# Kernel tuning notes

Measured on AMD Instinct MI355X. Metric: run time of the kernel, lower is better.

## Reference

```python
import jax, jax.numpy as jnp
import numpy as np

HEADS = 4
BN_EPS = 1e-5


def _hgat_conv(x, src, dst, node_type, edge_attr, edge_type,
               ne, W, We, a_src, a_dst, a_edge, ee, Wres, b, concat):
    """Heterogeneous GAT conv: per-type embeddings + edge-featured attention.
    x: [N, Fin]; edge_attr: [E, De]; returns [N, H*C] (concat) or [N, C]."""
    N = x.shape[0]
    C = W.shape[1] // HEADS
    xi = x + ne[node_type]                                  # node-type conditioning
    h = (xi @ W).reshape(N, HEADS, C)                       # [N, H, C]
    he = ((edge_attr + ee[edge_type]) @ We).reshape(-1, HEADS, C)  # [E, H, C]
    s = jnp.einsum('nhc,hc->nh', h, a_src)                  # [N, H]
    d = jnp.einsum('nhc,hc->nh', h, a_dst)                  # [N, H]
    e = jnp.einsum('ehc,hc->eh', he, a_edge)                # [E, H]
    alpha = jax.nn.leaky_relu(s[src] + d[dst] + e, 0.2)     # [E, H]
    # softmax over incoming edges per destination node
    amax = jax.ops.segment_max(alpha, dst, num_segments=N)  # [N, H]
    amax = jnp.where(jnp.isfinite(amax), amax, 0.0)
    ex = jnp.exp(alpha - amax[dst])
    den = jax.ops.segment_sum(ex, dst, num_segments=N)
    coef = ex / (den[dst] + 1e-16)                          # [E, H]
    msg = h[src] * coef[:, :, None]                         # [E, H, C]
    out = jax.ops.segment_sum(msg, dst, num_segments=N)     # [N, H, C]
    out = out.reshape(N, HEADS * C) if concat else out.mean(axis=1)
    return out + x @ Wres + b                               # residual + bias


def _batch_norm(x, gamma, beta):
    mu = x.mean(axis=0)
    var = x.var(axis=0)
    return (x - mu) * jax.lax.rsqrt(var + BN_EPS) * gamma + beta


def setup_inputs() -> dict:
    key = jax.random.key(0)
    ks = jax.random.split(key, 32)
    N, E, H = 50000, 400000, 32          # nodes, edges, hidden_channels
    DE = 64                               # edge_dim
    NT, ET = 3, 4                         # node / edge type counts
    D1 = H * HEADS                        # 128 = enc1 output / enc2 width

    def g(k, shape, scale=1.0):
        return (jax.random.normal(ks[k], shape, dtype=jnp.float32) * scale)

    inp = {
        'x': g(0, (N, H)),
        'edge_index': jax.random.randint(ks[1], (2, E), 0, N, dtype=jnp.int32),
        'node_type': jax.random.randint(ks[2], (N,), 0, NT, dtype=jnp.int32),
        'edge_attr': g(3, (E, DE)),
        'edge_type': jax.random.randint(ks[4], (E,), 0, ET, dtype=jnp.int32),
        # enc1 params (in=32, per-head out=32, concat -> 128)
        'ne1': g(5, (NT, H), 0.1),
        'w1': g(6, (H, HEADS * H), 1.0 / np.sqrt(H)),
        'we1': g(7, (DE, HEADS * H), 1.0 / np.sqrt(DE)),
        'asrc1': g(8, (HEADS, H), 0.1), 'adst1': g(9, (HEADS, H), 0.1),
        'aedge1': g(10, (HEADS, H), 0.1),
        'ee1': g(11, (ET, DE), 0.1),
        'wres1': g(12, (H, D1), 1.0 / np.sqrt(H)),
        'b1': jnp.zeros((D1,), jnp.float32),
        # BatchNorm(128)
        'gamma': jnp.ones((D1,), jnp.float32),
        'beta': jnp.zeros((D1,), jnp.float32),
        # enc2 params (in=128, per-head out=128, mean -> 128)
        'ne2': g(13, (NT, D1), 0.1),
        'w2': g(14, (D1, HEADS * D1), 1.0 / np.sqrt(D1)),
        'we2': g(15, (DE, HEADS * D1), 1.0 / np.sqrt(DE)),
        'asrc2': g(16, (HEADS, D1), 0.1), 'adst2': g(17, (HEADS, D1), 0.1),
        'aedge2': g(18, (HEADS, D1), 0.1),
        'ee2': g(19, (ET, DE), 0.1),
        'wres2': g(20, (D1, D1), 1.0 / np.sqrt(D1)),
        'b2': jnp.zeros((D1,), jnp.float32),
    }
    return inp


def reference(x, edge_index, node_type, edge_attr, edge_type,
              ne1, w1, we1, asrc1, adst1, aedge1, ee1, wres1, b1,
              gamma, beta,
              ne2, w2, we2, asrc2, adst2, aedge2, ee2, wres2, b2):
    src, dst = edge_index[0], edge_index[1]
    h = _hgat_conv(x, src, dst, node_type, edge_attr, edge_type,
                   ne1, w1, we1, asrc1, adst1, aedge1, ee1, wres1, b1,
                   concat=True)
    h = _batch_norm(h, gamma, beta)
    out = _hgat_conv(h, src, dst, node_type, edge_attr, edge_type,
                     ne2, w2, we2, asrc2, adst2, aedge2, ee2, wres2, b2,
                     concat=False)
    return out
```

## Files before the change

### kernel.cpp

```cpp
#include <hip/hip_runtime.h>
#include <hip/hip_bf16.h>

typedef unsigned short u16;
typedef unsigned int u32;

constexpr int NN = 50000;
constexpr int NE = 400000;
constexpr int MPAD = 50048;

typedef __attribute__((ext_vector_type(8))) short s16x8;
typedef __attribute__((ext_vector_type(4))) float f32x4;

__device__ __forceinline__ float bf2f(u16 u) {
    union { u32 i; float f; } v; v.i = ((u32)u) << 16; return v.f;
}
__device__ __forceinline__ u16 f2bf(float f) {
    union { float f; u32 i; } v; v.f = f;
    u32 r = v.i + 0x7fffu + ((v.i >> 16) & 1u);
    return (u16)(r >> 16);
}
__device__ __forceinline__ float ldf(const void* p, size_t i, int isbf) {
    if (isbf) return bf2f(((const u16*)p)[i]);
    return ((const float*)p)[i];
}
__device__ __forceinline__ float clampf(float v) {
    return fminf(fmaxf(v, -1e4f), 1e4f);
}

__device__ int   g_flag;
__device__ int   g_counter;
__device__ float g_qe1[256], g_qe2[256];
__device__ float g_eq1[16], g_eq2[16];
__device__ float g_ps1[128], g_pd1[128], g_ps2[512], g_pd2[512];
__device__ float g_bnsum[128], g_bnsumsq[128], g_bnscale[128], g_bnshift[128];
__device__ int   g_deg[NN], g_start[NN], g_cur[NN];
__device__ int   g_eidx[NE];
__device__ __attribute__((aligned(16))) float g_sbuf[NN * 4];
__device__ __attribute__((aligned(16))) float g_dbuf[NN * 4];
__device__ __attribute__((aligned(16))) float g_alpha[(size_t)NE * 4];
__device__ __attribute__((aligned(16))) float g_el2[(size_t)NE * 4];
__device__ __attribute__((aligned(16))) float g_xbuf[(size_t)NN * 128];
__device__ __attribute__((aligned(16))) float g_acc2[(size_t)NN * 128];
__device__ __attribute__((aligned(16))) u16 g_A1[(size_t)MPAD * 64];
__device__ __attribute__((aligned(16))) u16 g_A2[(size_t)MPAD * 160];
__device__ __attribute__((aligned(16))) u16 g_B1t[192 * 64];
__device__ __attribute__((aligned(16))) u16 g_B1bt[128 * 128];
__device__ __attribute__((aligned(16))) u16 g_B2t[192 * 160];
__device__ __attribute__((aligned(16))) u16 g_B2bt[128 * 512];
__device__ __attribute__((aligned(16))) u16 g_qeB[16 * 64];
__device__ __attribute__((aligned(16))) u16 g_xi1[(size_t)NN * 32];
__device__ __attribute__((aligned(16))) u16 g_xi2[(size_t)NN * 128];
__device__ __attribute__((aligned(16))) u16 g_agg1[(size_t)MPAD * 128];
__device__ __attribute__((aligned(16))) u16 g_agg2[(size_t)MPAD * 512];

__global__ void k_detect(const u16* x) {
    if (threadIdx.x == 0) {
        int cnt = 0;
        for (int i = 0; i < 64; i++) {
            u16 u = x[2 * i];
            int ex = (u >> 7) & 0xff;
            if (ex >= 100 && ex <= 140) cnt++;
        }
        g_flag = (cnt >= 40) ? 1 : 0;
        g_counter = 0;
    }
}
__global__ void k_zero() {
    int i = blockIdx.x * blockDim.x + threadIdx.x;
    if (i < NN) g_deg[i] = 0;
    if (i < 128) { g_bnsum[i] = 0.f; g_bnsumsq[i] = 0.f; }
}

__global__ __launch_bounds__(256) void k_prep(
    const void* we1, const void* ae1, const void* we2, const void* ae2,
    const void* w1, const void* as1, const void* ad1,
    const void* w2, const void* as2, const void* ad2) {
    int isbf = g_flag;
    int t = threadIdx.x;
    int idx = blockIdx.x * 16 + (t >> 4);
    int s = t & 15;
    float a = 0.f;
    if (idx < 256) {
        int k = idx >> 2, hd = idx & 3;
        for (int c = s; c < 32; c += 16)
            a += ldf(we1, k * 128 + hd * 32 + c, isbf) * ldf(ae1, hd * 32 + c, isbf);
    } else if (idx < 512) {
        int i2 = idx - 256;
        int k = i2 >> 2, hd = i2 & 3;
        for (int c = s; c < 128; c += 16)
            a += ldf(we2, k * 512 + hd * 128 + c, isbf) * ldf(ae2, hd * 128 + c, isbf);
    } else if (idx < 768) {
        int i2 = idx - 512;
        int isd = i2 >> 7, j = i2 & 127;
        int h = j >> 5, k = j & 31;
        const void* av = isd ? ad1 : as1;
        for (int c = s; c < 32; c += 16)
            a += ldf(w1, k * 128 + h * 32 + c, isbf) * ldf(av, h * 32 + c, isbf);
    } else {
        int i2 = idx - 768;
        int isd = i2 >> 9, j = i2 & 511;
        int h = j >> 7, k = j & 127;
        const void* av = isd ? ad2 : as2;
        for (int c = s; c < 128; c += 16)
            a += ldf(w2, (size_t)k * 512 + h * 128 + c, isbf) * ldf(av, h * 128 + c, isbf);
    }
#pragma unroll
    for (int mk = 8; mk >= 1; mk >>= 1) a += __shfl_xor(a, mk);
    if (s == 0) {
        if (idx < 256) g_qe1[idx] = a;
        else if (idx < 512) g_qe2[idx - 256] = a;
        else if (idx < 768) {
            int i2 = idx - 512;
            if (i2 >> 7) g_pd1[i2 & 127] = a; else g_ps1[i2 & 127] = a;
        } else {
            int i2 = idx - 768;
            if (i2 >> 9) g_pd2[i2 & 511] = a; else g_ps2[i2 & 511] = a;
        }
    }
}
__global__ void k_prep2(const void* ee1, const void* ee2) {
    int isbf = g_flag;
    int t = threadIdx.x;
    int idx = blockIdx.x * 16 + (t >> 4);
    int s = t & 15;
    int lyr = idx >> 4;
    int et = (idx >> 2) & 3, h = idx & 3;
    const void* ee = lyr ? ee2 : ee1;
    const float* qe = lyr ? g_qe2 : g_qe1;
    float a = 0.f;
    for (int k = s; k < 64; k += 16)
        a += ldf(ee, et * 64 + k, isbf) * qe[k * 4 + h];
#pragma unroll
    for (int mk = 8; mk >= 1; mk >>= 1) a += __shfl_xor(a, mk);
    if (s == 0) {
        if (lyr) g_eq2[et * 4 + h] = a; else g_eq1[et * 4 + h] = a;
    }
    int base = blockIdx.x * 256 + t;
    for (int i = base; i < 1024; i += 512) {
        int col = i >> 6, k = i & 63;
        float v = 0.f;
        if (col < 4) v = g_qe1[k * 4 + col];
        else if (col < 8) v = g_qe2[k * 4 + (col - 4)];
        g_qeB[col * 64 + k] = f2bf(v);
    }
}

__global__ void k_deg(const int* __restrict__ dstp) {
    int e = blockIdx.x * blockDim.x + threadIdx.x;
    if (e < NE) atomicAdd(&g_deg[dstp[e]], 1);
}
__global__ void k_start() {
    int n = blockIdx.x * blockDim.x + threadIdx.x;
    if (n < NN) {
        int d = g_deg[n];
        int s = atomicAdd(&g_counter, d);
        g_start[n] = s; g_cur[n] = s;
    }
}
__global__ void k_scatter(const int* __restrict__ dstp) {
    int e = blockIdx.x * blockDim.x + threadIdx.x;
    if (e < NE) {
        int slot = atomicAdd(&g_cur[dstp[e]], 1);
        g_eidx[slot] = e;
    }
}

__device__ __forceinline__ u16 a1val(const void* x, int n, int k, int nt, int isbf) {
    if (k < 32) return f2bf(ldf(x, (size_t)n * 32 + k, isbf));
    if (k == 32 + nt || k == 35) return 0x3F80u;
    return 0;
}
__global__ __launch_bounds__(256) void k_buildA1(const void* x, const int* __restrict__ ntype,
                                                 const void* ne1) {
    int isbf = g_flag;
    int i = blockIdx.x * 256 + threadIdx.x;
    if (i >= MPAD * 32) return;
    int n = i >> 5, k2 = (i & 31) << 1;
    u32 pk = 0;
    if (n < NN) {
        int nt = ntype[n];
        pk = (u32)a1val(x, n, k2, nt, isbf) | ((u32)a1val(x, n, k2 + 1, nt, isbf) << 16);
        if (k2 < 32) {
            float x0 = ldf(x, (size_t)n * 32 + k2, isbf) + ldf(ne1, nt * 32 + k2, isbf);
            float x1 = ldf(x, (size_t)n * 32 + k2 + 1, isbf) + ldf(ne1, nt * 32 + k2 + 1, isbf);
            ((u32*)g_xi1)[(size_t)n * 16 + (k2 >> 1)] =
                (u32)f2bf(x0) | ((u32)f2bf(x1) << 16);
        }
    }
    ((u32*)g_A1)[i] = pk;
}
__global__ __launch_bounds__(256) void k_a2tail(const int* __restrict__ ntype) {
    int i = blockIdx.x * 256 + threadIdx.x;
    if (i >= NN * 16) return;
    int n = i >> 4, q = i & 15;
    int k2 = 128 + q * 2;
    int nt = ntype[n];
    u16 lo = (k2 == 128 + nt || k2 == 131) ? 0x3F80u : 0;
    u16 hi = (k2 + 1 == 128 + nt || k2 + 1 == 131) ? 0x3F80u : 0;
    ((u32*)g_A2)[(size_t)n * 80 + 64 + q] = (u32)lo | ((u32)hi << 16);
}
__global__ __launch_bounds__(256) void k_xi2(const int* __restrict__ ntype, const void* ne2) {
    int isbf = g_flag;
    int i = blockIdx.x * 256 + threadIdx.x;
    if (i >= NN * 64) return;
    int n = i >> 6, jp = (i & 63) << 1;
    int nt = ntype[n];
    float v0 = g_xbuf[(size_t)n * 128 + jp] * g_bnscale[jp] + g_bnshift[jp]
             + ldf(ne2, nt * 128 + jp, isbf);
    float v1 = g_xbuf[(size_t)n * 128 + jp + 1] * g_bnscale[jp + 1] + g_bnshift[jp + 1]
             + ldf(ne2, nt * 128 + jp + 1, isbf);
    ((u32*)g_xi2)[i] = (u32)f2bf(v0) | ((u32)f2bf(v1) << 16);
}

__global__ void k_buildB1(const void* ne1, const void* w1, const void* wres1, const void* b1) {
    int isbf = g_flag;
    int j = blockIdx.x;
    int k = threadIdx.x;
    float v = 0.f;
    if (j < 128) {
        if (k < 32) v = ldf(wres1, k * 128 + j, isbf);
        else if (k == 35) v = ldf(b1, j, isbf);
    } else if (j < 136) {
        int h = (j - 128) & 3;
        const float* p = (j < 132) ? g_ps1 : g_pd1;
        if (k < 32) v = p[h * 32 + k];
        else if (k < 35) {
            int tt = k - 32; float a = 0.f;
            for (int c = 0; c < 32; c++)
                a += ldf(ne1, tt * 32 + c, isbf) * p[h * 32 + c];
            v = a;
        }
    }
    (void)w1;
    g_B1t[j * 64 + k] = f2bf(v);
}
__global__ void k_buildB1b(const void* w1) {
    int isbf = g_flag;
    int j = blockIdx.x;
    int k = threadIdx.x;
    float v = ((k >> 5) == (j >> 5)) ? ldf(w1, (k & 31) * 128 + j, isbf) : 0.f;
    g_B1bt[j * 128 + k] = f2bf(v);
}
__global__ void k_buildB2(const void* ne2, const void* w2, const void* wres2, const void* b2) {
    int isbf = g_flag;
    int j = blockIdx.x;
    int k = threadIdx.x;
    if (k >= 160) return;
    float v = 0.f;
    if (j < 128) {
        if (k < 128) v = g_bnscale[k] * ldf(wres2, k * 128 + j, isbf);
        else if (k == 131) {
            float a = ldf(b2, j, isbf);
            for (int c = 0; c < 128; c++)
                a += g_bnshift[c] * ldf(wres2, c * 128 + j, isbf);
            v = a;
        }
    } else if (j < 136) {
        int h = (j - 128) & 3;
        const float* p = (j < 132) ? g_ps2 : g_pd2;
        if (k < 128) v = g_bnscale[k] * p[h * 128 + k];
        else if (k < 131) {
            int tt = k - 128; float a = 0.f;
            for (int c = 0; c < 128; c++)
                a += (g_bnshift[c] + ldf(ne2, tt * 128 + c, isbf)) * p[h * 128 + c];
            v = a;
        }
    }
    (void)w2;
    g_B2t[j * 160 + k] = f2bf(v);
}
__global__ void k_buildB2b(const void* w2) {
    int isbf = g_flag;
    int j = blockIdx.x;
    for (int k = threadIdx.x; k < 512; k += 256) {
        float v = 0.25f * ldf(w2, (size_t)(k & 127) * 512 + (k >> 7) * 128 + j, isbf);
        g_B2bt[j * 512 + k] = f2bf(v);
    }
}

template<int K, int KT, int LAYER>
__global__ __launch_bounds__(256) void k_gemm(void* outp) {
    constexpr int KP = KT + 8;
    __shared__ __attribute__((aligned(16))) u16 As[64 * KP];
    __shared__ __attribute__((aligned(16))) u16 Bs[64 * KP];
    const u16* __restrict__ A  = (LAYER == 1) ? g_A1 : (LAYER == 2) ? g_A2
                               : (LAYER == 3) ? g_agg1 : g_agg2;
    const u16* __restrict__ Bt = (LAYER == 1) ? g_B1t : (LAYER == 2) ? g_B2t
                               : (LAYER == 3) ? g_B1bt : g_B2bt;
    int isbf = g_flag;
    const int t = threadIdx.x;
    const int mb = blockIdx.x, cb = blockIdx.y;
    const int wave = t >> 6, lane = t & 63;
    const int lr = lane & 15, lg = lane >> 4;
    f32x4 acc[4] = {};
    constexpr int CH = KT / 8;
#pragma unroll 1
    for (int kt = 0; kt < K / KT; kt++) {
        __syncthreads();
        for (int c = t; c < 64 * CH; c += 256) {
            int r = c / CH, o = (c - r * CH) * 8;
            *(s16x8*)&As[r * KP + o] =
                *(const s16x8*)&A[((size_t)(mb * 64 + r)) * K + kt * KT + o];
            *(s16x8*)&Bs[r * KP + o] =
                *(const s16x8*)&Bt[((size_t)(cb * 64 + r)) * K + kt * KT + o];
        }
        __syncthreads();
        const u16* ap  = &As[(wave * 16 + lr) * KP + lg * 8];
        const u16* bp0 = &Bs[lr * KP + lg * 8];
#pragma unroll
        for (int ks = 0; ks < KT / 32; ks++) {
            s16x8 af = *(const s16x8*)(ap + ks * 32);
#pragma unroll
            for (int ct = 0; ct < 4; ct++) {
                s16x8 bf = *(const s16x8*)(bp0 + ct * 16 * KP + ks * 32);
                acc[ct] = __builtin_amdgcn_mfma_f32_16x16x32_bf16(af, bf, acc[ct], 0, 0, 0);
            }
        }
    }
    const int rowb = mb * 64 + wave * 16 + lg * 4;
#pragma unroll
    for (int ct = 0; ct < 4; ct++) {
        int j = cb * 64 + ct * 16 + lr;
#pragma unroll
        for (int r = 0; r < 4; r++) {
            int n = rowb + r;
            if (n >= NN) continue;
            float v = acc[ct][r];
            if (LAYER == 1) {
                if (j < 128)      g_xbuf[(size_t)n * 128 + j] = clampf(v);
                else if (j < 132) g_sbuf[n * 4 + (j - 128)] = clampf(v);
                else if (j < 136) g_dbuf[n * 4 + (j - 132)] = clampf(v);
            } else if (LAYER == 2) {
                if (j < 128)      g_acc2[(size_t)n * 128 + j] = clampf(v);
                else if (j < 132) g_sbuf[n * 4 + (j - 128)] = clampf(v);
                else if (j < 136) g_dbuf[n * 4 + (j - 132)] = clampf(v);
            } else if (LAYER == 3) {
                float* p = &g_xbuf[(size_t)n * 128 + j];
                float x = clampf(*p + v);
                *p = x;
                g_A2[(size_t)n * 160 + j] = f2bf(x);
            } else {
                float v2 = clampf(g_acc2[(size_t)n * 128 + j] + v);
                if (isbf) ((u16*)outp)[(size_t)n * 128 + j] = f2bf(v2);
                else      ((float*)outp)[(size_t)n * 128 + j] = v2;
            }
        }
    }
}

__global__ __launch_bounds__(256) void k_edgemm(
    const int* __restrict__ etype, const void* eattr) {
    int isbf = g_flag;
    int t = threadIdx.x, wave = t >> 6, lane = t & 63;
    int lr = lane & 15, lg = lane >> 4;
    s16x8 bf0 = *(const s16x8*)&g_qeB[lr * 64 + lg * 8];
    s16x8 bf1 = *(const s16x8*)&g_qeB[lr * 64 + 32 + lg * 8];
    int ebase = blockIdx.x * 256 + wave * 64;
#pragma unroll 1
    for (int tile = 0; tile < 4; tile++) {
        int e0 = ebase + tile * 16;
        int ea = e0 + lr; if (ea >= NE) ea = NE - 1;
        f32x4 acc = {};
        if (isbf) {
            const u16* ep = (const u16*)eattr + (size_t)ea * 64 + lg * 8;
            s16x8 va = *(const s16x8*)(ep);
            s16x8 vb = *(const s16x8*)(ep + 32);
            acc = __builtin_amdgcn_mfma_f32_16x16x32_bf16(va, bf0, acc, 0, 0, 0);
            acc = __builtin_amdgcn_mfma_f32_16x16x32_bf16(vb, bf1, acc, 0, 0, 0);
        } else {
            const float* ep = (const float*)eattr + (size_t)ea * 64 + lg * 8;
            float4 fa = *(const float4*)(ep);
            float4 fb = *(const float4*)(ep + 4);
            float4 fc = *(const float4*)(ep + 32);
            float4 fd = *(const float4*)(ep + 36);
            s16x8 va, vb;
            va[0] = (short)f2bf(fa.x); va[1] = (short)f2bf(fa.y);
            va[2] = (short)f2bf(fa.z); va[3] = (short)f2bf(fa.w);
            va[4] = (short)f2bf(fb.x); va[5] = (short)f2bf(fb.y);
            va[6] = (short)f2bf(fb.z); va[7] = (short)f2bf(fb.w);
            vb[0] = (short)f2bf(fc.x); vb[1] = (short)f2bf(fc.y);
            vb[2] = (short)f2bf(fc.z); vb[3] = (short)f2bf(fc.w);
            vb[4] = (short)f2bf(fd.x); vb[5] = (short)f2bf(fd.y);
            vb[6] = (short)f2bf(fd.z); vb[7] = (short)f2bf(fd.w);
            acc = __builtin_amdgcn_mfma_f32_16x16x32_bf16(va, bf0, acc, 0, 0, 0);
            acc = __builtin_amdgcn_mfma_f32_16x16x32_bf16(vb, bf1, acc, 0, 0, 0);
        }
#pragma unroll
        for (int r = 0; r < 4; r++) {
            int ee = e0 + lg * 4 + r;
            int lb = lg * 16;
            float v0 = __shfl(acc[r], lb + 0), v1 = __shfl(acc[r], lb + 1);
            float v2 = __shfl(acc[r], lb + 2), v3 = __shfl(acc[r], lb + 3);
            float w0 = __shfl(acc[r], lb + 4), w1 = __shfl(acc[r], lb + 5);
            float w2 = __shfl(acc[r], lb + 6), w3 = __shfl(acc[r], lb + 7);
            if (ee < NE && (lr == 0 || lr == 4)) {
                int et = etype[ee];
                if (lr == 0) {
                    const float* q = g_eq1 + et * 4;
                    *(float4*)(g_alpha + 4 * (size_t)ee) = make_float4(
                        v0 + q[0], v1 + q[1], v2 + q[2], v3 + q[3]);
                } else {
                    const float* q = g_eq2 + et * 4;
                    *(float4*)(g_el2 + 4 * (size_t)ee) = make_float4(
                        w0 + q[0], w1 + q[1], w2 + q[2], w3 + q[3]);
                }
            }
        }
    }
}

__global__ __launch_bounds__(256) void k_edgeadd(
    const int* __restrict__ srcp, const int* __restrict__ dstp, int lyr) {
    int e = blockIdx.x * 256 + threadIdx.x;
    if (e >= NE) return;
    const float* el = (lyr == 1) ? g_alpha : g_el2;
    float4 p = *(const float4*)(el + 4 * (size_t)e);
    int ss = srcp[e], dd = dstp[e];
    float4 sb = *(const float4*)(g_sbuf + ss * 4);
    float4 db = *(const float4*)(g_dbuf + dd * 4);
    float a0 = sb.x + db.x + p.x;
    float a1 = sb.y + db.y + p.y;
    float a2 = sb.z + db.z + p.z;
    float a3 = sb.w + db.w + p.w;
    a0 = a0 > 0.f ? a0 : 0.2f * a0;
    a1 = a1 > 0.f ? a1 : 0.2f * a1;
    a2 = a2 > 0.f ? a2 : 0.2f * a2;
    a3 = a3 > 0.f ? a3 : 0.2f * a3;
    *(float4*)(g_alpha + 4 * (size_t)e) = make_float4(
        clampf(a0), clampf(a1), clampf(a2), clampf(a3));
}

__global__ __launch_bounds__(256) void k_att1(const int* __restrict__ srcp) {
    int lane = threadIdx.x & 63;
    int n = blockIdx.x * 4 + (threadIdx.x >> 6);
    if (n >= NN) return;
    int st = g_start[n], dg = g_deg[n];
    float m0 = -1e30f, m1 = -1e30f, m2 = -1e30f, m3 = -1e30f;
    for (int i = lane; i < dg; i += 64) {
        int e = g_eidx[st + i];
        float4 a = *(const float4*)(g_alpha + 4 * (size_t)e);
        m0 = fmaxf(m0, a.x); m1 = fmaxf(m1, a.y);
        m2 = fmaxf(m2, a.z); m3 = fmaxf(m3, a.w);
    }
    for (int mk = 32; mk >= 1; mk >>= 1) {
        m0 = fmaxf(m0, __shfl_xor(m0, mk)); m1 = fmaxf(m1, __shfl_xor(m1, mk));
        m2 = fmaxf(m2, __shfl_xor(m2, mk)); m3 = fmaxf(m3, __shfl_xor(m3, mk));
    }
    int j0 = 2 * lane;
    int hd = j0 >> 5;
    float z0 = 0.f, z1 = 0.f, z2 = 0.f, z3 = 0.f;
    float acc0 = 0.f, acc1 = 0.f;
    for (int base = 0; base < dg; base += 64) {
        int i = base + lane;
        int sidx = 0; float c0 = 0.f, c1 = 0.f, c2 = 0.f, c3 = 0.f;
        if (i < dg) {
            int e = g_eidx[st + i];
            float4 a = *(const float4*)(g_alpha + 4 * (size_t)e);
            sidx = srcp[e];
            c0 = expf(a.x - m0); c1 = expf(a.y - m1);
            c2 = expf(a.z - m2); c3 = expf(a.w - m3);
            z0 += c0; z1 += c1; z2 += c2; z3 += c3;
        }
        int cnt = min(64, dg - base);
        for (int jj = 0; jj < cnt; jj++) {
            int s2 = __shfl(sidx, jj);
            float b0 = __shfl(c0, jj), b1 = __shfl(c1, jj);
            float b2v = __shfl(c2, jj), b3 = __shfl(c3, jj);
            float cs = hd == 0 ? b0 : hd == 1 ? b1 : hd == 2 ? b2v : b3;
            u32 hv = *(const u32*)(g_xi1 + (size_t)s2 * 32 + (j0 & 31));
            acc0 += bf2f((u16)(hv & 0xffff)) * cs;
            acc1 += bf2f((u16)(hv >> 16)) * cs;
        }
    }
    for (int mk = 32; mk >= 1; mk >>= 1) {
        z0 += __shfl_xor(z0, mk); z1 += __shfl_xor(z1, mk);
        z2 += __shfl_xor(z2, mk); z3 += __shfl_xor(z3, mk);
    }
    float iv = 1.f / ((hd == 0 ? z0 : hd == 1 ? z1 : hd == 2 ? z2 : z3) + 1e-16f);
    ((u32*)g_agg1)[((size_t)n * 128 + j0) >> 1] =
        (u32)f2bf(acc0 * iv) | ((u32)f2bf(acc1 * iv) << 16);
}

__global__ __launch_bounds__(256) void k_bnstats() {
    int t = threadIdx.x;
    int j = t & 127;
    int r0 = blockIdx.x * 2 + (t >> 7);
    float s = 0.f, ss = 0.f;
    for (int r = r0; r < NN; r += 500) {
        float v = g_xbuf[(size_t)r * 128 + j];
        s += v; ss += v * v;
    }
    atomicAdd(&g_bnsum[j], s);
    atomicAdd(&g_bnsumsq[j], ss);
}
__global__ void k_bnfin(const void* gamma, const void* beta) {
    int isbf = g_flag;
    int j = threadIdx.x;
    float mu = g_bnsum[j] * (1.f / NN);
    float var = fmaxf(g_bnsumsq[j] * (1.f / NN) - mu * mu, 0.f);
    float rstd = rsqrtf(var + 1e-5f);
    float sc = ldf(gamma, j, isbf) * rstd;
    g_bnscale[j] = sc;
    g_bnshift[j] = ldf(beta, j, isbf) - mu * sc;
}

__global__ __launch_bounds__(256) void k_att2(const int* __restrict__ srcp) {
    int lane = threadIdx.x & 63;
    int n = blockIdx.x * 4 + (threadIdx.x >> 6);
    if (n >= NN) return;
    int st = g_start[n], dg = g_deg[n];
    float m0 = -1e30f, m1 = -1e30f, m2 = -1e30f, m3 = -1e30f;
    for (int i = lane; i < dg; i += 64) {
        int e = g_eidx[st + i];
        float4 a = *(const float4*)(g_alpha + 4 * (size_t)e);
        m0 = fmaxf(m0, a.x); m1 = fmaxf(m1, a.y);
        m2 = fmaxf(m2, a.z); m3 = fmaxf(m3, a.w);
    }
    for (int mk = 32; mk >= 1; mk >>= 1) {
        m0 = fmaxf(m0, __shfl_xor(m0, mk)); m1 = fmaxf(m1, __shfl_xor(m1, mk));
        m2 = fmaxf(m2, __shfl_xor(m2, mk)); m3 = fmaxf(m3, __shfl_xor(m3, mk));
    }
    int c0 = 2 * lane;
    float z0 = 0.f, z1 = 0.f, z2 = 0.f, z3 = 0.f;
    float a00 = 0.f, a01 = 0.f, a10 = 0.f, a11 = 0.f;
    float a20 = 0.f, a21 = 0.f, a30 = 0.f, a31 = 0.f;
    for (int base = 0; base < dg; base += 64) {
        int i = base + lane;
        int sidx = 0; float c0f = 0.f, c1f = 0.f, c2f = 0.f, c3f = 0.f;
        if (i < dg) {
            int e = g_eidx[st + i];
            float4 a = *(const float4*)(g_alpha + 4 * (size_t)e);
            sidx = srcp[e];
            c0f = expf(a.x - m0); c1f = expf(a.y - m1);
            c2f = expf(a.z - m2); c3f = expf(a.w - m3);
            z0 += c0f; z1 += c1f; z2 += c2f; z3 += c3f;
        }
        int cnt = min(64, dg - base);
        for (int jj = 0; jj < cnt; jj++) {
            int s2 = __shfl(sidx, jj);
            float b0 = __shfl(c0f, jj), b1 = __shfl(c1f, jj);
            float b2v = __shfl(c2f, jj), b3 = __shfl(c3f, jj);
            u32 hv = *(const u32*)(g_xi2 + (size_t)s2 * 128 + c0);
            float lo = bf2f((u16)(hv & 0xffff)), hi = bf2f((u16)(hv >> 16));
            a00 += lo * b0;  a01 += hi * b0;
            a10 += lo * b1;  a11 += hi * b1;
            a20 += lo * b2v; a21 += hi * b2v;
            a30 += lo * b3;  a31 += hi * b3;
        }
    }
    for (int mk = 32; mk >= 1; mk >>= 1) {
        z0 += __shfl_xor(z0, mk); z1 += __shfl_xor(z1, mk);
        z2 += __shfl_xor(z2, mk); z3 += __shfl_xor(z3, mk);
    }
    float iv0 = 1.f / (z0 + 1e-16f), iv1 = 1.f / (z1 + 1e-16f);
    float iv2 = 1.f / (z2 + 1e-16f), iv3 = 1.f / (z3 + 1e-16f);
    u32* out = (u32*)g_agg2 + (((size_t)n * 512 + c0) >> 1);
    out[0]   = (u32)f2bf(a00 * iv0) | ((u32)f2bf(a01 * iv0) << 16);
    out[64]  = (u32)f2bf(a10 * iv1) | ((u32)f2bf(a11 * iv1) << 16);
    out[128] = (u32)f2bf(a20 * iv2) | ((u32)f2bf(a21 * iv2) << 16);
    out[192] = (u32)f2bf(a30 * iv3) | ((u32)f2bf(a31 * iv3) << 16);
}

extern "C" void kernel_launch(void* const* d_in, const int* in_sizes, int n_in,
                              void* d_out, int out_size, void* d_ws, size_t ws_size,
                              hipStream_t stream) {
    const void* x     = d_in[0];
    const int* ei     = (const int*)d_in[1];
    const int* ntype  = (const int*)d_in[2];
    const void* eattr = d_in[3];
    const int* etype  = (const int*)d_in[4];
    const void* ne1   = d_in[5];
    const void* w1    = d_in[6];
    const void* we1   = d_in[7];
    const void* asrc1 = d_in[8];
    const void* adst1 = d_in[9];
    const void* aedge1= d_in[10];
    const void* ee1   = d_in[11];
    const void* wres1 = d_in[12];
    const void* b1    = d_in[13];
    const void* gamma = d_in[14];
    const void* beta  = d_in[15];
    const void* ne2   = d_in[16];
    const void* w2    = d_in[17];
    const void* we2   = d_in[18];
    const void* asrc2 = d_in[19];
    const void* adst2 = d_in[20];
    const void* aedge2= d_in[21];
    const void* ee2   = d_in[22];
    const void* wres2 = d_in[23];
    const void* b2    = d_in[24];
    (void)in_sizes; (void)n_in; (void)out_size; (void)d_ws; (void)ws_size;

    const int* srcp = ei;
    const int* dstp = ei + NE;

    k_detect<<<1, 64, 0, stream>>>((const u16*)x);
    k_zero<<<196, 256, 0, stream>>>();
    k_prep<<<112, 256, 0, stream>>>(we1, aedge1, we2, aedge2,
                                    w1, asrc1, adst1, w2, asrc2, adst2);
    k_prep2<<<2, 256, 0, stream>>>(ee1, ee2);
    k_deg<<<1563, 256, 0, stream>>>(dstp);
    k_start<<<196, 256, 0, stream>>>();
    k_scatter<<<1563, 256, 0, stream>>>(dstp);

    k_edgemm<<<(NE + 255) / 256, 256, 0, stream>>>(etype, eattr);

    k_buildA1<<<(MPAD * 32 + 255) / 256, 256, 0, stream>>>(x, ntype, ne1);
    k_buildB1<<<192, 64, 0, stream>>>(ne1, w1, wres1, b1);
    k_buildB1b<<<128, 128, 0, stream>>>(w1);
    k_gemm<64, 64, 1><<<dim3(MPAD / 64, 3), 256, 0, stream>>>(nullptr);
    k_edgeadd<<<1563, 256, 0, stream>>>(srcp, dstp, 1);
    k_att1<<<12500, 256, 0, stream>>>(srcp);
    k_gemm<128, 128, 3><<<dim3(MPAD / 64, 2), 256, 0, stream>>>(nullptr);

    k_bnstats<<<250, 256, 0, stream>>>();
    k_bnfin<<<1, 128, 0, stream>>>(gamma, beta);

    k_xi2<<<12500, 256, 0, stream>>>(ntype, ne2);
    k_a2tail<<<(NN * 16 + 255) / 256, 256, 0, stream>>>(ntype);
    k_buildB2<<<192, 192, 0, stream>>>(ne2, w2, wres2, b2);
    k_buildB2b<<<128, 256, 0, stream>>>(w2);
    k_gemm<160, 160, 2><<<dim3(MPAD / 64, 3), 256, 0, stream>>>(nullptr);
    k_edgeadd<<<1563, 256, 0, stream>>>(srcp, dstp, 2);
    k_att2<<<12500, 256, 0, stream>>>(srcp);
    k_gemm<512, 128, 4><<<dim3(MPAD / 64, 2), 256, 0, stream>>>(d_out);
}
```

Before: 595.6 us.

## Write attention logits in CSR order with atomic segment max and fuse small kernels

The edge-add kernel now stores each edge's attention logits directly at its CSR slot and updates a per-destination max through order-preserving integer atomicMax. The attention kernels then read logits and source indices contiguously and skip the separate max pass and the edge-index indirection. Several small setup kernels are merged (detect+zero, a2tail+xi2, B1/B1b, B2/B2b) to cut launch count. The cost is 1.6M extra atomics, which can contend on high-degree nodes, plus an extra slot array and a re-zeroing of the max keys between layers.

```diff
diff --git a/kernel.cpp b/kernel.cpp
--- a/kernel.cpp
+++ b/kernel.cpp
@@ -25,6 +25,16 @@
 }
 __device__ __forceinline__ float clampf(float v) {
     return fminf(fmaxf(v, -1e4f), 1e4f);
+}
+__device__ __forceinline__ u32 menc(float f) {
+    union { float f; u32 i; } v; v.f = f;
+    return (v.i & 0x80000000u) ? ~v.i : (v.i | 0x80000000u);
+}
+__device__ __forceinline__ float mdec(u32 k) {
+    if (k == 0u) return 0.f;
+    union { u32 i; float f; } v;
+    v.i = (k & 0x80000000u) ? (k & 0x7fffffffu) : ~k;
+    return v.f;
 }
 
 __device__ int   g_flag;
@@ -34,11 +44,14 @@
 __device__ float g_ps1[128], g_pd1[128], g_ps2[512], g_pd2[512];
 __device__ float g_bnsum[128], g_bnsumsq[128], g_bnscale[128], g_bnshift[128];
 __device__ int   g_deg[NN], g_start[NN], g_cur[NN];
-__device__ int   g_eidx[NE];
+__device__ int   g_slot[NE];
+__device__ int   g_srccsr[NE];
+__device__ u32   g_mkey[NN * 4];
 __device__ __attribute__((aligned(16))) float g_sbuf[NN * 4];
 __device__ __attribute__((aligned(16))) float g_dbuf[NN * 4];
 __device__ __attribute__((aligned(16))) float g_alpha[(size_t)NE * 4];
 __device__ __attribute__((aligned(16))) float g_el2[(size_t)NE * 4];
+__device__ __attribute__((aligned(16))) float g_acsr[(size_t)NE * 4];
 __device__ __attribute__((aligned(16))) float g_xbuf[(size_t)NN * 128];
 __device__ __attribute__((aligned(16))) float g_acc2[(size_t)NN * 128];
 __device__ __attribute__((aligned(16))) u16 g_A1[(size_t)MPAD * 64];
@@ -53,22 +66,21 @@
 __device__ __attribute__((aligned(16))) u16 g_agg1[(size_t)MPAD * 128];
 __device__ __attribute__((aligned(16))) u16 g_agg2[(size_t)MPAD * 512];
 
-__global__ void k_detect(const u16* x) {
-    if (threadIdx.x == 0) {
+__global__ void k_zero(const u16* x) {
+    int i = blockIdx.x * blockDim.x + threadIdx.x;
+    if (i < NN) g_deg[i] = 0;
+    if (i < NN * 4) g_mkey[i] = 0u;
+    if (i < 128) { g_bnsum[i] = 0.f; g_bnsumsq[i] = 0.f; }
+    if (i == 0) {
         int cnt = 0;
-        for (int i = 0; i < 64; i++) {
-            u16 u = x[2 * i];
+        for (int j = 0; j < 64; j++) {
+            u16 u = x[2 * j];
             int ex = (u >> 7) & 0xff;
             if (ex >= 100 && ex <= 140) cnt++;
         }
         g_flag = (cnt >= 40) ? 1 : 0;
         g_counter = 0;
     }
-}
-__global__ void k_zero() {
-    int i = blockIdx.x * blockDim.x + threadIdx.x;
-    if (i < NN) g_deg[i] = 0;
-    if (i < 128) { g_bnsum[i] = 0.f; g_bnsumsq[i] = 0.f; }
 }
 
 __global__ __launch_bounds__(256) void k_prep(
@@ -157,11 +169,12 @@
         g_start[n] = s; g_cur[n] = s;
     }
 }
-__global__ void k_scatter(const int* __restrict__ dstp) {
+__global__ void k_scatter(const int* __restrict__ srcp, const int* __restrict__ dstp) {
     int e = blockIdx.x * blockDim.x + threadIdx.x;
     if (e < NE) {
         int slot = atomicAdd(&g_cur[dstp[e]], 1);
-        g_eidx[slot] = e;
+        g_slot[e] = slot;
+        g_srccsr[slot] = srcp[e];
     }
 }
 
@@ -189,19 +202,18 @@
     }
     ((u32*)g_A1)[i] = pk;
 }
-__global__ __launch_bounds__(256) void k_a2tail(const int* __restrict__ ntype) {
+__global__ __launch_bounds__(256) void k_xi2(const int* __restrict__ ntype, const void* ne2) {
+    int isbf = g_flag;
     int i = blockIdx.x * 256 + threadIdx.x;
-    if (i >= NN * 16) return;
-    int n = i >> 4, q = i & 15;
-    int k2 = 128 + q * 2;
-    int nt = ntype[n];
-    u16 lo = (k2 == 128 + nt || k2 == 131) ? 0x3F80u : 0;
-    u16 hi = (k2 + 1 == 128 + nt || k2 + 1 == 131) ? 0x3F80u : 0;
-    ((u32*)g_A2)[(size_t)n * 80 + 64 + q] = (u32)lo | ((u32)hi << 16);
-}
-__global__ __launch_bounds__(256) void k_xi2(const int* __restrict__ ntype, const void* ne2) {
-    int isbf = g_flag;
-    int i = blockIdx.x * 256 + threadIdx.x;
+    if (i < NN * 4) g_mkey[i] = 0u;
+    if (i < NN * 16) {
+        int n = i >> 4, q = i & 15;
+        int k2 = 128 + q * 2;
+        int nt = ntype[n];
+        u16 lo = (k2 == 128 + nt || k2 == 131) ? 0x3F80u : 0;
+        u16 hi = (k2 + 1 == 128 + nt || k2 + 1 == 131) ? 0x3F80u : 0;
+        ((u32*)g_A2)[(size_t)n * 80 + 64 + q] = (u32)lo | ((u32)hi << 16);
+    }
     if (i >= NN * 64) return;
     int n = i >> 6, jp = (i & 63) << 1;
     int nt = ntype[n];
@@ -212,69 +224,71 @@
     ((u32*)g_xi2)[i] = (u32)f2bf(v0) | ((u32)f2bf(v1) << 16);
 }
 
-__global__ void k_buildB1(const void* ne1, const void* w1, const void* wres1, const void* b1) {
-    int isbf = g_flag;
-    int j = blockIdx.x;
+__global__ void k_buildB1all(const void* ne1, const void* w1,
+                             const void* wres1, const void* b1) {
+    int isbf = g_flag;
+    int bj = blockIdx.x;
     int k = threadIdx.x;
-    float v = 0.f;
-    if (j < 128) {
-        if (k < 32) v = ldf(wres1, k * 128 + j, isbf);
-        else if (k == 35) v = ldf(b1, j, isbf);
-    } else if (j < 136) {
-        int h = (j - 128) & 3;
-        const float* p = (j < 132) ? g_ps1 : g_pd1;
-        if (k < 32) v = p[h * 32 + k];
-        else if (k < 35) {
-            int tt = k - 32; float a = 0.f;
-            for (int c = 0; c < 32; c++)
-                a += ldf(ne1, tt * 32 + c, isbf) * p[h * 32 + c];
-            v = a;
-        }
-    }
-    (void)w1;
-    g_B1t[j * 64 + k] = f2bf(v);
-}
-__global__ void k_buildB1b(const void* w1) {
-    int isbf = g_flag;
-    int j = blockIdx.x;
+    if (bj < 192) {
+        if (k >= 64) return;
+        int j = bj;
+        float v = 0.f;
+        if (j < 128) {
+            if (k < 32) v = ldf(wres1, k * 128 + j, isbf);
+            else if (k == 35) v = ldf(b1, j, isbf);
+        } else if (j < 136) {
+            int h = (j - 128) & 3;
+            const float* p = (j < 132) ? g_ps1 : g_pd1;
+            if (k < 32) v = p[h * 32 + k];
+            else if (k < 35) {
+                int tt = k - 32; float a = 0.f;
+                for (int c = 0; c < 32; c++)
+                    a += ldf(ne1, tt * 32 + c, isbf) * p[h * 32 + c];
+                v = a;
+            }
+        }
+        g_B1t[j * 64 + k] = f2bf(v);
+    } else {
+        int j = bj - 192;
+        float v = ((k >> 5) == (j >> 5)) ? ldf(w1, (k & 31) * 128 + j, isbf) : 0.f;
+        g_B1bt[j * 128 + k] = f2bf(v);
+    }
+}
+__global__ void k_buildB2all(const void* ne2, const void* w2,
+                             const void* wres2, const void* b2) {
+    int isbf = g_flag;
+    int bj = blockIdx.x;
     int k = threadIdx.x;
-    float v = ((k >> 5) == (j >> 5)) ? ldf(w1, (k & 31) * 128 + j, isbf) : 0.f;
-    g_B1bt[j * 128 + k] = f2bf(v);
-}
-__global__ void k_buildB2(const void* ne2, const void* w2, const void* wres2, const void* b2) {
-    int isbf = g_flag;
-    int j = blockIdx.x;
-    int k = threadIdx.x;
-    if (k >= 160) return;
-    float v = 0.f;
-    if (j < 128) {
-        if (k < 128) v = g_bnscale[k] * ldf(wres2, k * 128 + j, isbf);
-        else if (k == 131) {
-            float a = ldf(b2, j, isbf);
-            for (int c = 0; c < 128; c++)
-                a += g_bnshift[c] * ldf(wres2, c * 128 + j, isbf);
-            v = a;
-        }
-    } else if (j < 136) {
-        int h = (j - 128) & 3;
-        const float* p = (j < 132) ? g_ps2 : g_pd2;
-        if (k < 128) v = g_bnscale[k] * p[h * 128 + k];
-        else if (k < 131) {
-            int tt = k - 128; float a = 0.f;
-            for (int c = 0; c < 128; c++)
-                a += (g_bnshift[c] + ldf(ne2, tt * 128 + c, isbf)) * p[h * 128 + c];
-            v = a;
-        }
-    }
-    (void)w2;
-    g_B2t[j * 160 + k] = f2bf(v);
-}
-__global__ void k_buildB2b(const void* w2) {
-    int isbf = g_flag;
-    int j = blockIdx.x;
-    for (int k = threadIdx.x; k < 512; k += 256) {
-        float v = 0.25f * ldf(w2, (size_t)(k & 127) * 512 + (k >> 7) * 128 + j, isbf);
-        g_B2bt[j * 512 + k] = f2bf(v);
+    if (bj < 192) {
+        if (k >= 160) return;
+        int j = bj;
+        float v = 0.f;
+        if (j < 128) {
+            if (k < 128) v = g_bnscale[k] * ldf(wres2, k * 128 + j, isbf);
+            else if (k == 131) {
+                float a = ldf(b2, j, isbf);
+                for (int c = 0; c < 128; c++)
+                    a += g_bnshift[c] * ldf(wres2, c * 128 + j, isbf);
+                v = a;
+            }
+        } else if (j < 136) {
+            int h = (j - 128) & 3;
+            const float* p = (j < 132) ? g_ps2 : g_pd2;
+            if (k < 128) v = g_bnscale[k] * p[h * 128 + k];
+            else if (k < 131) {
+                int tt = k - 128; float a = 0.f;
+                for (int c = 0; c < 128; c++)
+                    a += (g_bnshift[c] + ldf(ne2, tt * 128 + c, isbf)) * p[h * 128 + c];
+                v = a;
+            }
+        }
+        g_B2t[j * 160 + k] = f2bf(v);
+    } else {
+        int j = bj - 192;
+        for (int kk = k; kk < 512; kk += 256) {
+            float v = 0.25f * ldf(w2, (size_t)(kk & 127) * 512 + (kk >> 7) * 128 + j, isbf);
+            g_B2bt[j * 512 + kk] = f2bf(v);
+        }
     }
 }
 
@@ -422,30 +436,26 @@
     float a1 = sb.y + db.y + p.y;
     float a2 = sb.z + db.z + p.z;
     float a3 = sb.w + db.w + p.w;
-    a0 = a0 > 0.f ? a0 : 0.2f * a0;
-    a1 = a1 > 0.f ? a1 : 0.2f * a1;
-    a2 = a2 > 0.f ? a2 : 0.2f * a2;
-    a3 = a3 > 0.f ? a3 : 0.2f * a3;
-    *(float4*)(g_alpha + 4 * (size_t)e) = make_float4(
-        clampf(a0), clampf(a1), clampf(a2), clampf(a3));
-}
-
-__global__ __launch_bounds__(256) void k_att1(const int* __restrict__ srcp) {
+    a0 = clampf(a0 > 0.f ? a0 : 0.2f * a0);
+    a1 = clampf(a1 > 0.f ? a1 : 0.2f * a1);
+    a2 = clampf(a2 > 0.f ? a2 : 0.2f * a2);
+    a3 = clampf(a3 > 0.f ? a3 : 0.2f * a3);
+    int slot = g_slot[e];
+    *(float4*)(g_acsr + 4 * (size_t)slot) = make_float4(a0, a1, a2, a3);
+    u32* mk = &g_mkey[dd * 4];
+    atomicMax(&mk[0], menc(a0));
+    atomicMax(&mk[1], menc(a1));
+    atomicMax(&mk[2], menc(a2));
+    atomicMax(&mk[3], menc(a3));
+}
+
+__global__ __launch_bounds__(256) void k_att1() {
     int lane = threadIdx.x & 63;
     int n = blockIdx.x * 4 + (threadIdx.x >> 6);
     if (n >= NN) return;
     int st = g_start[n], dg = g_deg[n];
-    float m0 = -1e30f, m1 = -1e30f, m2 = -1e30f, m3 = -1e30f;
-    for (int i = lane; i < dg; i += 64) {
-        int e = g_eidx[st + i];
-        float4 a = *(const float4*)(g_alpha + 4 * (size_t)e);
-        m0 = fmaxf(m0, a.x); m1 = fmaxf(m1, a.y);
-        m2 = fmaxf(m2, a.z); m3 = fmaxf(m3, a.w);
-    }
-    for (int mk = 32; mk >= 1; mk >>= 1) {
-        m0 = fmaxf(m0, __shfl_xor(m0, mk)); m1 = fmaxf(m1, __shfl_xor(m1, mk));
-        m2 = fmaxf(m2, __shfl_xor(m2, mk)); m3 = fmaxf(m3, __shfl_xor(m3, mk));
-    }
+    uint4 mk = *(const uint4*)&g_mkey[n * 4];
+    float m0 = mdec(mk.x), m1 = mdec(mk.y), m2 = mdec(mk.z), m3 = mdec(mk.w);
     int j0 = 2 * lane;
     int hd = j0 >> 5;
     float z0 = 0.f, z1 = 0.f, z2 = 0.f, z3 = 0.f;
@@ -454,9 +464,8 @@
         int i = base + lane;
         int sidx = 0; float c0 = 0.f, c1 = 0.f, c2 = 0.f, c3 = 0.f;
         if (i < dg) {
-            int e = g_eidx[st + i];
-            float4 a = *(const float4*)(g_alpha + 4 * (size_t)e);
-            sidx = srcp[e];
+            float4 a = *(const float4*)(g_acsr + 4 * (size_t)(st + i));
+            sidx = g_srccsr[st + i];
             c0 = expf(a.x - m0); c1 = expf(a.y - m1);
             c2 = expf(a.z - m2); c3 = expf(a.w - m3);
             z0 += c0; z1 += c1; z2 += c2; z3 += c3;
@@ -472,9 +481,9 @@
             acc1 += bf2f((u16)(hv >> 16)) * cs;
         }
     }
-    for (int mk = 32; mk >= 1; mk >>= 1) {
-        z0 += __shfl_xor(z0, mk); z1 += __shfl_xor(z1, mk);
-        z2 += __shfl_xor(z2, mk); z3 += __shfl_xor(z3, mk);
+    for (int mk2 = 32; mk2 >= 1; mk2 >>= 1) {
+        z0 += __shfl_xor(z0, mk2); z1 += __shfl_xor(z1, mk2);
+        z2 += __shfl_xor(z2, mk2); z3 += __shfl_xor(z3, mk2);
     }
     float iv = 1.f / ((hd == 0 ? z0 : hd == 1 ? z1 : hd == 2 ? z2 : z3) + 1e-16f);
     ((u32*)g_agg1)[((size_t)n * 128 + j0) >> 1] =
@@ -504,22 +513,13 @@
     g_bnshift[j] = ldf(beta, j, isbf) - mu * sc;
 }
 
-__global__ __launch_bounds__(256) void k_att2(const int* __restrict__ srcp) {
+__global__ __launch_bounds__(256) void k_att2() {
     int lane = threadIdx.x & 63;
     int n = blockIdx.x * 4 + (threadIdx.x >> 6);
     if (n >= NN) return;
     int st = g_start[n], dg = g_deg[n];
-    float m0 = -1e30f, m1 = -1e30f, m2 = -1e30f, m3 = -1e30f;
-    for (int i = lane; i < dg; i += 64) {
-        int e = g_eidx[st + i];
-        float4 a = *(const float4*)(g_alpha + 4 * (size_t)e);
-        m0 = fmaxf(m0, a.x); m1 = fmaxf(m1, a.y);
-        m2 = fmaxf(m2, a.z); m3 = fmaxf(m3, a.w);
-    }
-    for (int mk = 32; mk >= 1; mk >>= 1) {
-        m0 = fmaxf(m0, __shfl_xor(m0, mk)); m1 = fmaxf(m1, __shfl_xor(m1, mk));
-        m2 = fmaxf(m2, __shfl_xor(m2, mk)); m3 = fmaxf(m3, __shfl_xor(m3, mk));
-    }
+    uint4 mk = *(const uint4*)&g_mkey[n * 4];
+    float m0 = mdec(mk.x), m1 = mdec(mk.y), m2 = mdec(mk.z), m3 = mdec(mk.w);
     int c0 = 2 * lane;
     float z0 = 0.f, z1 = 0.f, z2 = 0.f, z3 = 0.f;
     float a00 = 0.f, a01 = 0.f, a10 = 0.f, a11 = 0.f;
@@ -528,9 +528,8 @@
         int i = base + lane;
         int sidx = 0; float c0f = 0.f, c1f = 0.f, c2f = 0.f, c3f = 0.f;
         if (i < dg) {
-            int e = g_eidx[st + i];
-            float4 a = *(const float4*)(g_alpha + 4 * (size_t)e);
-            sidx = srcp[e];
+            float4 a = *(const float4*)(g_acsr + 4 * (size_t)(st + i));
+            sidx = g_srccsr[st + i];
             c0f = expf(a.x - m0); c1f = expf(a.y - m1);
             c2f = expf(a.z - m2); c3f = expf(a.w - m3);
             z0 += c0f; z1 += c1f; z2 += c2f; z3 += c3f;
@@ -548,9 +547,9 @@
             a30 += lo * b3;  a31 += hi * b3;
         }
     }
-    for (int mk = 32; mk >= 1; mk >>= 1) {
-        z0 += __shfl_xor(z0, mk); z1 += __shfl_xor(z1, mk);
-        z2 += __shfl_xor(z2, mk); z3 += __shfl_xor(z3, mk);
+    for (int mk2 = 32; mk2 >= 1; mk2 >>= 1) {
+        z0 += __shfl_xor(z0, mk2); z1 += __shfl_xor(z1, mk2);
+        z2 += __shfl_xor(z2, mk2); z3 += __shfl_xor(z3, mk2);
     }
     float iv0 = 1.f / (z0 + 1e-16f), iv1 = 1.f / (z1 + 1e-16f);
     float iv2 = 1.f / (z2 + 1e-16f), iv3 = 1.f / (z3 + 1e-16f);
@@ -594,34 +593,30 @@
     const int* srcp = ei;
     const int* dstp = ei + NE;
 
-    k_detect<<<1, 64, 0, stream>>>((const u16*)x);
-    k_zero<<<196, 256, 0, stream>>>();
+    k_zero<<<(NN * 4 + 255) / 256, 256, 0, stream>>>((const u16*)x);
     k_prep<<<112, 256, 0, stream>>>(we1, aedge1, we2, aedge2,
                                     w1, asrc1, adst1, w2, asrc2, adst2);
     k_prep2<<<2, 256, 0, stream>>>(ee1, ee2);
     k_deg<<<1563, 256, 0, stream>>>(dstp);
     k_start<<<196, 256, 0, stream>>>();
-    k_scatter<<<1563, 256, 0, stream>>>(dstp);
+    k_scatter<<<1563, 256, 0, stream>>>(srcp, dstp);
 
     k_edgemm<<<(NE + 255) / 256, 256, 0, stream>>>(etype, eattr);
 
     k_buildA1<<<(MPAD * 32 + 255) / 256, 256, 0, stream>>>(x, ntype, ne1);
-    k_buildB1<<<192, 64, 0, stream>>>(ne1, w1, wres1, b1);
-    k_buildB1b<<<128, 128, 0, stream>>>(w1);
+    k_buildB1all<<<320, 128, 0, stream>>>(ne1, w1, wres1, b1);
     k_gemm<64, 64, 1><<<dim3(MPAD / 64, 3), 256, 0, stream>>>(nullptr);
     k_edgeadd<<<1563, 256, 0, stream>>>(srcp, dstp, 1);
-    k_att1<<<12500, 256, 0, stream>>>(srcp);
+    k_att1<<<12500, 256, 0, stream>>>();
     k_gemm<128, 128, 3><<<dim3(MPAD / 64, 2), 256, 0, stream>>>(nullptr);
 
     k_bnstats<<<250, 256, 0, stream>>>();
     k_bnfin<<<1, 128, 0, stream>>>(gamma, beta);
 
     k_xi2<<<12500, 256, 0, stream>>>(ntype, ne2);
-    k_a2tail<<<(NN * 16 + 255) / 256, 256, 0, stream>>>(ntype);
-    k_buildB2<<<192, 192, 0, stream>>>(ne2, w2, wres2, b2);
-    k_buildB2b<<<128, 256, 0, stream>>>(w2);
+    k_buildB2all<<<320, 256, 0, stream>>>(ne2, w2, wres2, b2);
     k_gemm<160, 160, 2><<<dim3(MPAD / 64, 3), 256, 0, stream>>>(nullptr);
     k_edgeadd<<<1563, 256, 0, stream>>>(srcp, dstp, 2);
-    k_att2<<<12500, 256, 0, stream>>>(srcp);
+    k_att2<<<12500, 256, 0, stream>>>();
     k_gemm<512, 128, 4><<<dim3(MPAD / 64, 2), 256, 0, stream>>>(d_out);
 }
```

After: 692.2 us. 1.16x slower.
